# Optimization experiments

Hardware: AMD Instinct MI355X
Metric: run time of the kernel (lower is better)

The kernel has to match this reference:

```python
import jax, jax.numpy as jnp
import numpy as np

B, T, C, H, FF, BOT = 2, 2048, 1024, 16, 4096, 64
D = C // H
EPS = 1e-5

def _ln(x, g, b):
    m = jnp.mean(x, axis=-1, keepdims=True)
    v = jnp.mean(jnp.square(x - m), axis=-1, keepdims=True)
    return (x - m) * jax.lax.rsqrt(v + EPS) * g + b

def setup_inputs() -> dict:
    key = jax.random.key(0)
    ks = jax.random.split(key, 20)
    def lin(k, fan_in, shape):
        return jax.random.normal(k, shape, jnp.float32) * (1.0 / np.sqrt(fan_in))
    inp = {
        "x": jax.random.normal(ks[0], (B, T, C), jnp.float32),
        # causal mask: masked_fill where mask == 0
        "attn_mask": jnp.tril(jnp.ones((T, T), jnp.int32))[None, None, :, :],
        "Wq": lin(ks[1], C, (C, C)), "bq": jnp.zeros((C,), jnp.float32),
        "Wk": lin(ks[2], C, (C, C)), "bk": jnp.zeros((C,), jnp.float32),
        "Wv": lin(ks[3], C, (C, C)), "bv": jnp.zeros((C,), jnp.float32),
        "Wo": lin(ks[4], C, (C, C)), "bo": jnp.zeros((C,), jnp.float32),
        "g1": jnp.ones((C,), jnp.float32), "beta1": jnp.zeros((C,), jnp.float32),
        "g2": jnp.ones((C,), jnp.float32), "beta2": jnp.zeros((C,), jnp.float32),
        "W1": lin(ks[5], C, (C, FF)), "bf1": jnp.zeros((FF,), jnp.float32),
        "W2": lin(ks[6], FF, (FF, C)), "bf2": jnp.zeros((C,), jnp.float32),
        "Wd": lin(ks[7], C, (C, BOT)), "bd": jnp.zeros((BOT,), jnp.float32),
        "Wu": lin(ks[8], BOT, (BOT, C)), "bu": jnp.zeros((C,), jnp.float32),
    }
    return inp

def reference(x, attn_mask, Wq, bq, Wk, bk, Wv, bv, Wo, bo,
              g1, beta1, g2, beta2, W1, bf1, W2, bf2, Wd, bd, Wu, bu):
    # --- attention sublayer ---
    xn = _ln(x, g1, beta1)
    q = (xn @ Wq + bq).reshape(B, T, H, D)
    k = (xn @ Wk + bk).reshape(B, T, H, D)
    v = (xn @ Wv + bv).reshape(B, T, H, D)
    scores = jnp.einsum('bthd,bshd->bhts', q, k) / jnp.sqrt(jnp.float32(D))
    scores = jnp.where(attn_mask == 0, -jnp.inf, scores)
    w = jax.nn.softmax(scores, axis=-1)
    attn = jnp.einsum('bhts,bshd->bthd', w, v).reshape(B, T, C)
    x = x + attn @ Wo + bo
    # --- FFN + adapter sublayer ---
    xn2 = _ln(x, g2, beta2)
    h = jax.nn.relu(xn2 @ W1 + bf1) @ W2 + bf2
    h = h + jax.nn.relu(h @ Wd + bd) @ Wu + bu  # adapter residual
    return x + h
```

## Files before the change

kernel.cpp:

```cpp
#include <hip/hip_runtime.h>
#include <cstdint>
#include <cstddef>

typedef unsigned short u16;
typedef __attribute__((ext_vector_type(4))) short short4v;
typedef __attribute__((ext_vector_type(8))) short short8;
typedef __attribute__((ext_vector_type(4))) float f32x4;

__device__ __forceinline__ float bf2f(u16 h) { return __uint_as_float(((unsigned)h) << 16); }
__device__ __forceinline__ u16 f2bf(float f) {
    unsigned u = __float_as_uint(f);
    unsigned r = (u + 0x7fffu + ((u >> 16) & 1u)) >> 16;
    return (u16)r;
}
__device__ __forceinline__ u16 f2bf_fast(float f) {
    return (u16)((__float_as_uint(f) + 0x8000u) >> 16);
}

__device__ __forceinline__ void gl_lds16(const void* g, void* l) {
    __builtin_amdgcn_global_load_lds((const __attribute__((address_space(1))) void*)g,
                                     (__attribute__((address_space(3))) void*)l, 16, 0, 0);
}

struct Prologue {
    const void* tsrc[8];
    u16* tdst[8];
    int tR[8], tC[8], toff[8];
    const void* psrc[12];
    int poff[12], pn[12];
    int ntrans;
};
__global__ __launch_bounds__(256) void prologue_kernel(Prologue P,
                                                       const unsigned* __restrict__ x,
                                                       int* __restrict__ flag,
                                                       float* __restrict__ pf) {
    __shared__ int cnt[256];
    int c = 0;
    for (int i = threadIdx.x; i < 1024; i += 256) {
        unsigned lo = x[i] & 0xFFFFu;
        unsigned e = (lo >> 7) & 0xFFu;
        c += (e >= 100u && e <= 150u) ? 1 : 0;
    }
    cnt[threadIdx.x] = c;
    __syncthreads();
    for (int s = 128; s > 0; s >>= 1) {
        if (threadIdx.x < s) cnt[threadIdx.x] += cnt[threadIdx.x + s];
        __syncthreads();
    }
    const int bf = (cnt[0] > 512) ? 1 : 0;
    if (blockIdx.x == 0 && threadIdx.x == 0) *flag = bf;

    const int bid = blockIdx.x;
    if (bid >= P.ntrans) {
        const int s = bid - P.ntrans;
        const void* sp = P.psrc[s];
        float* dp = pf + P.poff[s];
        const int n = P.pn[s];
        for (int i = threadIdx.x; i < n; i += 256)
            dp[i] = bf ? bf2f(((const u16*)sp)[i]) : ((const float*)sp)[i];
        return;
    }
    __shared__ u16 tile[32][33];
    int m = 0;
#pragma unroll
    for (int i = 1; i < 8; i++) m = (bid >= P.toff[i]) ? i : m;
    const int local = bid - P.toff[m];
    const int R = P.tR[m], C = P.tC[m];
    const int tilesx = C >> 5;
    const int bx = local % tilesx, by = local / tilesx;
    const void* src = P.tsrc[m];
    u16* dst = P.tdst[m];
    const int tx = threadIdx.x & 31, ty = threadIdx.x >> 5;
#pragma unroll
    for (int i = 0; i < 32; i += 8) {
        size_t idx = (size_t)(by * 32 + ty + i) * C + bx * 32 + tx;
        tile[ty + i][tx] = bf ? ((const u16*)src)[idx] : f2bf(((const float*)src)[idx]);
    }
    __syncthreads();
#pragma unroll
    for (int i = 0; i < 32; i += 8)
        dst[(size_t)(bx * 32 + ty + i) * R + by * 32 + tx] = tile[tx][ty + i];
}

__global__ __launch_bounds__(256) void ln_x_kernel(const void* __restrict__ X,
                                                   const float* __restrict__ G,
                                                   const float* __restrict__ Be,
                                                   u16* __restrict__ Xb,
                                                   u16* __restrict__ Y,
                                                   const int* __restrict__ flag) {
    const int row = blockIdx.x;
    const int tid = threadIdx.x;
    const int lane = tid & 63, wave = tid >> 6;
    u16 vbuf[4];
    if (*flag) {
        *(uint2*)vbuf = *(const uint2*)((const u16*)X + (size_t)row * 1024 + tid * 4);
    } else {
        float4 v = *(const float4*)((const float*)X + (size_t)row * 1024 + tid * 4);
        vbuf[0] = f2bf(v.x); vbuf[1] = f2bf(v.y); vbuf[2] = f2bf(v.z); vbuf[3] = f2bf(v.w);
    }
    *(uint2*)&Xb[(size_t)row * 1024 + tid * 4] = *(uint2*)vbuf;
    float f[4];
    float s = 0.f, sq = 0.f;
#pragma unroll
    for (int j = 0; j < 4; j++) { f[j] = bf2f(vbuf[j]); s += f[j]; sq += f[j] * f[j]; }
#pragma unroll
    for (int m = 1; m < 64; m <<= 1) { s += __shfl_xor(s, m, 64); sq += __shfl_xor(sq, m, 64); }
    __shared__ float rs_[4], rq_[4];
    if (lane == 0) { rs_[wave] = s; rq_[wave] = sq; }
    __syncthreads();
    float S = rs_[0] + rs_[1] + rs_[2] + rs_[3];
    float Q2 = rq_[0] + rq_[1] + rq_[2] + rq_[3];
    float mean = S * (1.f / 1024.f);
    float var = Q2 * (1.f / 1024.f) - mean * mean;
    float rstd = rsqrtf(var + 1e-5f);
    u16 o[4];
#pragma unroll
    for (int j = 0; j < 4; j++) {
        int c2 = tid * 4 + j;
        float y = (f[j] - mean) * rstd * G[c2] + Be[c2];
        o[j] = f2bf(y);
    }
    *(uint2*)&Y[(size_t)row * 1024 + tid * 4] = *(uint2*)o;
}

__global__ __launch_bounds__(256) void ln_kernel(const u16* __restrict__ X,
                                                 const float* __restrict__ G,
                                                 const float* __restrict__ Be,
                                                 u16* __restrict__ Y) {
    const int row = blockIdx.x;
    const int tid = threadIdx.x;
    const int lane = tid & 63, wave = tid >> 6;
    const u16* xr = X + (size_t)row * 1024;
    u16 vbuf[4];
    *(uint2*)vbuf = *(const uint2*)&xr[tid * 4];
    float f[4];
    float s = 0.f, sq = 0.f;
#pragma unroll
    for (int j = 0; j < 4; j++) { f[j] = bf2f(vbuf[j]); s += f[j]; sq += f[j] * f[j]; }
#pragma unroll
    for (int m = 1; m < 64; m <<= 1) { s += __shfl_xor(s, m, 64); sq += __shfl_xor(sq, m, 64); }
    __shared__ float rs_[4], rq_[4];
    if (lane == 0) { rs_[wave] = s; rq_[wave] = sq; }
    __syncthreads();
    float S = rs_[0] + rs_[1] + rs_[2] + rs_[3];
    float Q2 = rq_[0] + rq_[1] + rq_[2] + rq_[3];
    float mean = S * (1.f / 1024.f);
    float var = Q2 * (1.f / 1024.f) - mean * mean;
    float rstd = rsqrtf(var + 1e-5f);
    u16 o[4];
#pragma unroll
    for (int j = 0; j < 4; j++) {
        int c2 = tid * 4 + j;
        float y = (f[j] - mean) * rstd * G[c2] + Be[c2];
        o[j] = f2bf(y);
    }
    *(uint2*)&Y[(size_t)row * 1024 + tid * 4] = *(uint2*)o;
}

template <int TAG>
__global__ __launch_bounds__(512, 4) void gemm128_kernel(const u16* __restrict__ A,
                                                         const u16* __restrict__ Bt,
                                                         const float* __restrict__ bias,
                                                         const u16* __restrict__ res1,
                                                         const u16* __restrict__ res2,
                                                         void* __restrict__ out,
                                                         void* __restrict__ out_k,
                                                         void* __restrict__ out_v,
                                                         int M, int N, int K, int relu, int mode,
                                                         int swz,
                                                         const int* __restrict__ flag) {
    (void)flag; (void)M;
    __shared__ __align__(16) u16 As[2][2][128 * 32];
    __shared__ __align__(16) u16 Bs[2][2][128 * 32];
    const int tid = threadIdx.x;
    const int wave = tid >> 6, lane = tid & 63;
    const int l15 = lane & 15, quad = lane >> 4;
    const int wr = wave & 3, wc = wave >> 2;
    int bx = blockIdx.x, by = blockIdx.y;
    if (swz) {
        const int gx = gridDim.x;
        const int nwg = gx * gridDim.y;
        const int bid = by * gx + bx;
        const int sbid = (bid & 7) * (nwg >> 3) + (bid >> 3);
        bx = sbid % gx;
        by = sbid / gx;
    }
    const int m0 = by * 128, n0 = bx * 128;
    const int nt = K >> 6;

    const int rsub = lane >> 2;
    const int logc = (lane & 3) ^ ((rsub >> 1) & 3);

    auto stage_pair = [&](int t, int kh) {
        const int buf = t & 1;
        const int kk = (t << 6) + (kh << 5) + logc * 8;
        const int roff = wave * 16 + rsub;
        gl_lds16(A + (size_t)(m0 + roff) * K + kk, &As[buf][kh][wave * 512 + lane * 8]);
        gl_lds16(Bt + (size_t)(n0 + roff) * K + kk, &Bs[buf][kh][wave * 512 + lane * 8]);
    };

    f32x4 acc[2][4];
#pragma unroll
    for (int i = 0; i < 2; i++)
#pragma unroll
        for (int j = 0; j < 4; j++) acc[i][j] = (f32x4){0.f, 0.f, 0.f, 0.f};

    stage_pair(0, 0);
    stage_pair(0, 1);
    stage_pair(1, 0);
    asm volatile("s_waitcnt vmcnt(4)" ::: "memory");
    __builtin_amdgcn_s_barrier();

    const int rx = (l15 >> 1) & 3;
    for (int t = 0; t < nt; t++) {
        const int b = t & 1;
#pragma unroll
        for (int ph = 0; ph < 2; ph++) {
            const int kh = ph;
            short8 af[2], bfr[4];
#pragma unroll
            for (int i = 0; i < 2; i++)
                af[i] = *(const short8*)&As[b][kh][(wr * 32 + i * 16 + l15) * 32 +
                                                   ((quad ^ rx) << 3)];
#pragma unroll
            for (int j = 0; j < 4; j++)
                bfr[j] = *(const short8*)&Bs[b][kh][(wc * 64 + j * 16 + l15) * 32 +
                                                    ((quad ^ rx) << 3)];
            if (ph == 0) { if (t + 1 < nt) stage_pair(t + 1, 1); }
            else         { if (t + 2 < nt) stage_pair(t + 2, 0); }
            __builtin_amdgcn_s_setprio(1);
#pragma unroll
            for (int i = 0; i < 2; i++)
#pragma unroll
                for (int j = 0; j < 4; j++)
                    acc[i][j] = __builtin_amdgcn_mfma_f32_16x16x32_bf16(
                        af[i], bfr[j], acc[i][j], 0, 0, 0);
            __builtin_amdgcn_s_setprio(0);
            if (ph == 0) {
                if (t + 1 < nt) { asm volatile("s_waitcnt vmcnt(4)" ::: "memory"); }
                else            { asm volatile("s_waitcnt vmcnt(0)" ::: "memory"); }
            } else {
                if (t + 2 < nt)      { asm volatile("s_waitcnt vmcnt(4)" ::: "memory"); }
                else if (t + 1 < nt) { asm volatile("s_waitcnt vmcnt(2)" ::: "memory"); }
            }
            __builtin_amdgcn_s_barrier();
        }
    }

    if (mode == 2) {
        const int region = n0 >> 10;
        if (region < 2) {
            u16* o = (u16*)(region == 0 ? out : out_k);
#pragma unroll
            for (int j = 0; j < 4; j++) {
                const int col = n0 + wc * 64 + j * 16 + l15;
                const float bv = bias[col];
                const int cl = col & 1023;
#pragma unroll
                for (int i = 0; i < 2; i++) {
                    const int row0 = m0 + wr * 32 + i * 16 + quad * 4;
#pragma unroll
                    for (int r = 0; r < 4; r++)
                        o[(size_t)(row0 + r) * 1024 + cl] = f2bf(acc[i][j][r] + bv);
                }
            }
        } else {
            u16* o = (u16*)out_v;
#pragma unroll
            for (int j = 0; j < 4; j++) {
                const int col = n0 + wc * 64 + j * 16 + l15;
                const float bv = bias[col];
                const int cl = col & 1023;
                const int h = cl >> 6, d = cl & 63;
#pragma unroll
                for (int i = 0; i < 2; i++) {
                    const int row_base = m0 + wr * 32 + i * 16 + quad * 4;
                    const int bb = row_base >> 11, tt = row_base & 2047;
                    u16 pk[4];
#pragma unroll
                    for (int r = 0; r < 4; r++) pk[r] = f2bf(acc[i][j][r] + bv);
                    *(uint2*)&o[(((size_t)bb * 16 + h) * 64 + d) * 2048 + tt] = *(uint2*)pk;
                }
            }
        }
        return;
    }
#pragma unroll
    for (int j = 0; j < 4; j++) {
        const int col = n0 + wc * 64 + j * 16 + l15;
        const float bv = bias ? bias[col] : 0.f;
#pragma unroll
        for (int i = 0; i < 2; i++) {
            const int row0 = m0 + wr * 32 + i * 16 + quad * 4;
#pragma unroll
            for (int r = 0; r < 4; r++) {
                float v = acc[i][j][r] + bv;
                if (relu) v = fmaxf(v, 0.f);
                const size_t idx = (size_t)(row0 + r) * N + col;
                if (res1) v += bf2f(res1[idx]);
                if (res2) v += bf2f(res2[idx]);
                ((u16*)out)[idx] = f2bf(v);
            }
        }
    }
}

template <int TAG>
__global__ __launch_bounds__(512, 2) void gemm256w_kernel(const u16* __restrict__ A,
                                                          const u16* __restrict__ Bt,
                                                          const float* __restrict__ bias,
                                                          void* __restrict__ out,
                                                          int N, int K, int relu) {
    __shared__ __align__(16) u16 As[2][2][256 * 32];
    __shared__ __align__(16) u16 Bs[2][2][256 * 32];
    const int tid = threadIdx.x;
    const int wave = tid >> 6, lane = tid & 63;
    const int l15 = lane & 15, quad = lane >> 4;
    const int wr = wave >> 2, wc = wave & 3;
    const int m0 = blockIdx.y * 256, n0 = blockIdx.x * 256;
    const int nt = K >> 6;

    const int rsub = lane >> 2;
    const int logc = (lane & 3) ^ ((rsub >> 1) & 3);

    auto stage_pair = [&](int t, int kh) {
        const int buf = t & 1;
        const int kk = (t << 6) + (kh << 5) + logc * 8;
        const int r0 = wave * 32 + rsub;
        u16* da = &As[buf][kh][wave * 1024 + lane * 8];
        u16* db = &Bs[buf][kh][wave * 1024 + lane * 8];
        gl_lds16(A + (size_t)(m0 + r0) * K + kk, da);
        gl_lds16(A + (size_t)(m0 + r0 + 16) * K + kk, da + 512);
        gl_lds16(Bt + (size_t)(n0 + r0) * K + kk, db);
        gl_lds16(Bt + (size_t)(n0 + r0 + 16) * K + kk, db + 512);
    };

    f32x4 acc[8][4];
#pragma unroll
    for (int i = 0; i < 8; i++)
#pragma unroll
        for (int j = 0; j < 4; j++) acc[i][j] = (f32x4){0.f, 0.f, 0.f, 0.f};

    stage_pair(0, 0);
    stage_pair(0, 1);
    stage_pair(1, 0);
    asm volatile("s_waitcnt vmcnt(8)" ::: "memory");
    __builtin_amdgcn_s_barrier();

    const int rx = (l15 >> 1) & 3;
    for (int t = 0; t < nt; t++) {
        const int b = t & 1;
#pragma unroll
        for (int ph = 0; ph < 2; ph++) {
            const int kh = ph;
            short8 af[8], bfr[4];
#pragma unroll
            for (int i = 0; i < 8; i++)
                af[i] = *(const short8*)&As[b][kh][(wr * 128 + i * 16 + l15) * 32 +
                                                   ((quad ^ rx) << 3)];
#pragma unroll
            for (int j = 0; j < 4; j++)
                bfr[j] = *(const short8*)&Bs[b][kh][(wc * 64 + j * 16 + l15) * 32 +
                                                    ((quad ^ rx) << 3)];
            if (ph == 0) { if (t + 1 < nt) stage_pair(t + 1, 1); }
            else         { if (t + 2 < nt) stage_pair(t + 2, 0); }
            __builtin_amdgcn_s_setprio(1);
#pragma unroll
            for (int i = 0; i < 8; i++)
#pragma unroll
                for (int j = 0; j < 4; j++)
                    acc[i][j] = __builtin_amdgcn_mfma_f32_16x16x32_bf16(
                        af[i], bfr[j], acc[i][j], 0, 0, 0);
            __builtin_amdgcn_s_setprio(0);
            if (ph == 0) {
                if (t + 1 < nt) { asm volatile("s_waitcnt vmcnt(8)" ::: "memory"); }
                else            { asm volatile("s_waitcnt vmcnt(0)" ::: "memory"); }
            } else {
                if (t + 2 < nt)      { asm volatile("s_waitcnt vmcnt(8)" ::: "memory"); }
                else if (t + 1 < nt) { asm volatile("s_waitcnt vmcnt(4)" ::: "memory"); }
            }
            __builtin_amdgcn_s_barrier();
        }
    }

#pragma unroll
    for (int j = 0; j < 4; j++) {
        const int col = n0 + wc * 64 + j * 16 + l15;
        const float bv = bias ? bias[col] : 0.f;
#pragma unroll
        for (int i = 0; i < 8; i++) {
            const int row0 = m0 + wr * 128 + i * 16 + quad * 4;
#pragma unroll
            for (int r = 0; r < 4; r++) {
                float v = acc[i][j][r] + bv;
                if (relu) v = fmaxf(v, 0.f);
                ((u16*)out)[(size_t)(row0 + r) * N + col] = f2bf(v);
            }
        }
    }
}

template <int TAG>
__global__ __launch_bounds__(512, 2) void gemm128d_kernel(const u16* __restrict__ A,
                                                          const u16* __restrict__ Bt,
                                                          const float* __restrict__ bias,
                                                          const u16* __restrict__ res1,
                                                          void* __restrict__ out,
                                                          int N, int K, int relu, int swz) {
    __shared__ __align__(16) u16 As[2][2][128 * 64];
    __shared__ __align__(16) u16 Bs[2][2][128 * 64];
    const int tid = threadIdx.x;
    const int wave = tid >> 6, lane = tid & 63;
    const int l15 = lane & 15, quad = lane >> 4;
    const int wr = wave & 3, wc = wave >> 2;
    int bx = blockIdx.x, by = blockIdx.y;
    if (swz) {
        const int gx = gridDim.x;
        const int nwg = gx * gridDim.y;
        const int bid = by * gx + bx;
        const int sbid = (bid & 7) * (nwg >> 3) + (bid >> 3);
        bx = sbid % gx;
        by = sbid / gx;
    }
    const int m0 = by * 128, n0 = bx * 128;
    const int nt = K >> 7;

    const int srow = lane >> 3;
    const int logc = (lane & 7) ^ ((lane >> 4) & 3);

    auto stage_pair = [&](int t, int kh) {
        const int buf = t & 1;
        const int kk = (t << 7) + (kh << 6) + logc * 8;
        const int r0 = wave * 16 + srow;
        u16* da = &As[buf][kh][wave * 1024 + lane * 8];
        u16* db = &Bs[buf][kh][wave * 1024 + lane * 8];
        gl_lds16(A + (size_t)(m0 + r0) * K + kk, da);
        gl_lds16(A + (size_t)(m0 + r0 + 8) * K + kk, da + 512);
        gl_lds16(Bt + (size_t)(n0 + r0) * K + kk, db);
        gl_lds16(Bt + (size_t)(n0 + r0 + 8) * K + kk, db + 512);
    };

    f32x4 acc[2][4];
#pragma unroll
    for (int i = 0; i < 2; i++)
#pragma unroll
        for (int j = 0; j < 4; j++) acc[i][j] = (f32x4){0.f, 0.f, 0.f, 0.f};

    stage_pair(0, 0);
    stage_pair(0, 1);
    stage_pair(1, 0);
    asm volatile("s_waitcnt vmcnt(8)" ::: "memory");
    __builtin_amdgcn_s_barrier();

    const int rx = (l15 >> 1) & 3;
    for (int t = 0; t < nt; t++) {
        const int b = t & 1;
#pragma unroll
        for (int ph = 0; ph < 2; ph++) {
            const int kh = ph;
            short8 af[2][2], bfr[4][2];
#pragma unroll
            for (int ks = 0; ks < 2; ks++) {
                const int ck = ((ks << 2) | (quad ^ rx)) << 3;
#pragma unroll
                for (int i = 0; i < 2; i++)
                    af[i][ks] = *(const short8*)&As[b][kh][(wr * 32 + i * 16 + l15) * 64 + ck];
#pragma unroll
                for (int j = 0; j < 4; j++)
                    bfr[j][ks] = *(const short8*)&Bs[b][kh][(wc * 64 + j * 16 + l15) * 64 + ck];
            }
            if (ph == 0) { if (t + 1 < nt) stage_pair(t + 1, 1); }
            else         { if (t + 2 < nt) stage_pair(t + 2, 0); }
            __builtin_amdgcn_s_setprio(1);
#pragma unroll
            for (int ks = 0; ks < 2; ks++)
#pragma unroll
                for (int i = 0; i < 2; i++)
#pragma unroll
                    for (int j = 0; j < 4; j++)
                        acc[i][j] = __builtin_amdgcn_mfma_f32_16x16x32_bf16(
                            af[i][ks], bfr[j][ks], acc[i][j], 0, 0, 0);
            __builtin_amdgcn_s_setprio(0);
            if (ph == 0) {
                if (t + 1 < nt) { asm volatile("s_waitcnt vmcnt(8)" ::: "memory"); }
                else            { asm volatile("s_waitcnt vmcnt(0)" ::: "memory"); }
            } else {
                if (t + 2 < nt)      { asm volatile("s_waitcnt vmcnt(8)" ::: "memory"); }
                else if (t + 1 < nt) { asm volatile("s_waitcnt vmcnt(4)" ::: "memory"); }
            }
            __builtin_amdgcn_s_barrier();
        }
    }

#pragma unroll
    for (int j = 0; j < 4; j++) {
        const int col = n0 + wc * 64 + j * 16 + l15;
        const float bv = bias ? bias[col] : 0.f;
#pragma unroll
        for (int i = 0; i < 2; i++) {
            const int row0 = m0 + wr * 32 + i * 16 + quad * 4;
#pragma unroll
            for (int r = 0; r < 4; r++) {
                float v = acc[i][j][r] + bv;
                if (relu) v = fmaxf(v, 0.f);
                const size_t idx = (size_t)(row0 + r) * N + col;
                if (res1) v += bf2f(res1[idx]);
                ((u16*)out)[idx] = f2bf(v);
            }
        }
    }
}

__global__ __launch_bounds__(512) void adapter_kernel(const u16* __restrict__ hh,
                                                      const u16* __restrict__ x1,
                                                      const u16* __restrict__ WdT,
                                                      const u16* __restrict__ WuT,
                                                      const float* __restrict__ bd,
                                                      const float* __restrict__ bu,
                                                      void* __restrict__ out,
                                                      const int* __restrict__ flag) {
    const int tid = threadIdx.x;
    const int wave = tid >> 6, lane = tid & 63;
    const int l15 = lane & 15, quad = lane >> 4;
    const int r0 = blockIdx.x * 16;

    __shared__ float part[8][16 * 64];
    __shared__ __align__(16) u16 bot_s[16 * 72];

    f32x4 dacc[4];
#pragma unroll
    for (int j = 0; j < 4; j++) dacc[j] = (f32x4){0.f, 0.f, 0.f, 0.f};
    const int kw = wave * 128;
#pragma unroll
    for (int ks = 0; ks < 4; ks++) {
        const int k0 = kw + ks * 32 + quad * 8;
        short8 af = *(const short8*)&hh[(size_t)(r0 + l15) * 1024 + k0];
#pragma unroll
        for (int j = 0; j < 4; j++) {
            short8 bf = *(const short8*)&WdT[(size_t)(j * 16 + l15) * 1024 + k0];
            dacc[j] = __builtin_amdgcn_mfma_f32_16x16x32_bf16(af, bf, dacc[j], 0, 0, 0);
        }
    }
#pragma unroll
    for (int j = 0; j < 4; j++)
#pragma unroll
        for (int r = 0; r < 4; r++)
            part[wave][(quad * 4 + r) * 64 + j * 16 + l15] = dacc[j][r];
    __syncthreads();

    for (int e = tid; e < 1024; e += 512) {
        float s = part[0][e];
#pragma unroll
        for (int w = 1; w < 8; w++) s += part[w][e];
        s += bd[e & 63];
        s = fmaxf(s, 0.f);
        bot_s[(e >> 6) * 72 + (e & 63)] = f2bf(s);
    }
    __syncthreads();

    short8 auf[2];
    auf[0] = *(const short8*)&bot_s[l15 * 72 + quad * 8];
    auf[1] = *(const short8*)&bot_s[l15 * 72 + 32 + quad * 8];
    f32x4 uacc[8];
#pragma unroll
    for (int j = 0; j < 8; j++) uacc[j] = (f32x4){0.f, 0.f, 0.f, 0.f};
#pragma unroll
    for (int j = 0; j < 8; j++) {
        const size_t nb = (size_t)(wave * 128 + j * 16 + l15) * 64;
        short8 b0 = *(const short8*)&WuT[nb + quad * 8];
        short8 b1 = *(const short8*)&WuT[nb + 32 + quad * 8];
        uacc[j] = __builtin_amdgcn_mfma_f32_16x16x32_bf16(auf[0], b0, uacc[j], 0, 0, 0);
        uacc[j] = __builtin_amdgcn_mfma_f32_16x16x32_bf16(auf[1], b1, uacc[j], 0, 0, 0);
    }
    const int f32out = (*flag == 0);
#pragma unroll
    for (int j = 0; j < 8; j++) {
        const int col = wave * 128 + j * 16 + l15;
        const float bv = bu[col];
#pragma unroll
        for (int r = 0; r < 4; r++) {
            const int row = r0 + quad * 4 + r;
            const size_t idx = (size_t)row * 1024 + col;
            float v = uacc[j][r] + bv;
            v += bf2f(hh[idx]);
            v += bf2f(x1[idx]);
            if (f32out) ((float*)out)[idx] = v;
            else ((u16*)out)[idx] = f2bf(v);
        }
    }
}

template <int SPLIT>
__global__ __launch_bounds__(256) void flash_kernel(const u16* __restrict__ Q,
                                                    const u16* __restrict__ Kg,
                                                    const u16* __restrict__ VtG,
                                                    u16* __restrict__ O,
                                                    u16* __restrict__ pO,
                                                    float* __restrict__ pL) {
    const int tid = threadIdx.x;
    const int wave = tid >> 6, lane = tid & 63;
    int qb, ch;
    if (SPLIT) {
        const int i = blockIdx.x;
        if (i < 32)      { qb = 31 - (i >> 2); ch = i & 3; }
        else if (i < 56) { const int j = i - 32; qb = 23 - j / 3; ch = j % 3; }
        else if (i < 72) { const int j = i - 56; qb = 15 - (j >> 1); ch = j & 1; }
        else             { qb = 7 - (i - 72); ch = 0; }
    } else {
        qb = 31 - blockIdx.x; ch = 0;
    }
    const int bh = blockIdx.y;
    const int t0 = qb * 64;
    const int steps = qb + 1;
    const int ktbeg = SPLIT ? ch * 8 : 0;
    const int ktend = SPLIT ? (steps < ktbeg + 8 ? steps : ktbeg + 8) : steps;
    const size_t base = ((size_t)(bh >> 4) * 2048) * 1024 + (size_t)(bh & 15) * 64;
    const size_t basev = (size_t)bh * 64 * 2048;

    __shared__ __align__(16) u16 Ks[2][64 * 64];
    __shared__ __align__(16) u16 Vt[2][64 * 64];
#if !__has_builtin(__builtin_amdgcn_mfma_f32_16x16x16bf16_1k)
    __shared__ __align__(16) u16 Ps[4][16 * 72];
#endif

    const int l15 = lane & 15, quad = lane >> 4;
    const int rmin = t0 + wave * 16;

    short8 qf[2];
    {
        const u16* qp = Q + base + (size_t)(rmin + l15) * 1024 + quad * 8;
        qf[0] = *(const short8*)qp;
        qf[1] = *(const short8*)(qp + 32);
    }

    const int slr = lane >> 3;
    const int sc8 = (lane & 7) ^ slr;
    const int rb = wave * 16;

    auto stage = [&](int kt, int bufi) {
        gl_lds16(Kg + base + (size_t)(kt * 64 + rb + slr) * 1024 + sc8 * 8,
                 &Ks[bufi][rb * 64 + lane * 8]);
        gl_lds16(Kg + base + (size_t)(kt * 64 + rb + 8 + slr) * 1024 + sc8 * 8,
                 &Ks[bufi][(rb + 8) * 64 + lane * 8]);
        gl_lds16(VtG + basev + (size_t)(rb + slr) * 2048 + kt * 64 + sc8 * 8,
                 &Vt[bufi][rb * 64 + lane * 8]);
        gl_lds16(VtG + basev + (size_t)(rb + 8 + slr) * 2048 + kt * 64 + sc8 * 8,
                 &Vt[bufi][(rb + 8) * 64 + lane * 8]);
    };

    float l_part = 0.f;
    f32x4 oacc[4];
#pragma unroll
    for (int jt = 0; jt < 4; jt++) oacc[jt] = (f32x4){0.f, 0.f, 0.f, 0.f};

    const float Cs = 0.125f * 1.44269504f;

    stage(ktbeg, 0);
    __syncthreads();

    for (int kt = ktbeg; kt < ktend; kt++) {
        const int cur = kt & 1;
        if (kt + 1 < ktend) stage(kt + 1, cur ^ 1);

        short8 kf[2][4];
#pragma unroll
        for (int st = 0; st < 2; st++)
#pragma unroll
            for (int j = 0; j < 4; j++)
                kf[st][j] = *(const short8*)&Ks[cur][(j * 16 + l15) * 64 +
                                                     (((st * 4 + quad) ^ (l15 & 7)) * 8)];
#if __has_builtin(__builtin_amdgcn_mfma_f32_16x16x16bf16_1k)
        short4v vf[4][4];
#pragma unroll
        for (int j = 0; j < 4; j++) {
            int k8 = j * 2 + (quad >> 1);
#pragma unroll
            for (int jt = 0; jt < 4; jt++) {
                int d = jt * 16 + l15;
                vf[j][jt] = *(const short4v*)&Vt[cur][d * 64 + ((k8 ^ (d & 7)) * 8) +
                                                      (quad & 1) * 4];
            }
        }
#else
        short8 vf[2][4];
#pragma unroll
        for (int st = 0; st < 2; st++)
#pragma unroll
            for (int jt = 0; jt < 4; jt++) {
                int d = jt * 16 + l15;
                vf[st][jt] = *(const short8*)&Vt[cur][d * 64 + (((st * 4 + quad) ^ (d & 7)) * 8)];
            }
#endif

        f32x4 s[4];
#pragma unroll
        for (int j = 0; j < 4; j++) s[j] = (f32x4){0.f, 0.f, 0.f, 0.f};
#pragma unroll
        for (int st = 0; st < 2; st++)
#pragma unroll
            for (int j = 0; j < 4; j++)
                s[j] = __builtin_amdgcn_mfma_f32_16x16x32_bf16(kf[st][j], qf[st], s[j], 0, 0, 0);

        float lpv[4] = {0.f, 0.f, 0.f, 0.f};
        short4v pj[4];
        if (kt != qb) {
#pragma unroll
            for (int j = 0; j < 4; j++) {
                union { short4v v; u16 u[4]; } pk;
#pragma unroll
                for (int r = 0; r < 4; r++) {
                    float p = __builtin_amdgcn_exp2f(s[j][r] * Cs);
                    lpv[r] += p;
                    pk.u[r] = f2bf_fast(p);
                }
                pj[j] = pk.v;
            }
        } else {
            const int qrow = rmin + l15;
#pragma unroll
            for (int j = 0; j < 4; j++) {
                union { short4v v; u16 u[4]; } pk;
#pragma unroll
                for (int r = 0; r < 4; r++) {
                    float p = __builtin_amdgcn_exp2f(s[j][r] * Cs);
                    int key = kt * 64 + j * 16 + quad * 4 + r;
                    if (key > qrow) p = 0.f;
                    lpv[r] += p;
                    pk.u[r] = f2bf_fast(p);
                }
                pj[j] = pk.v;
            }
        }
        l_part += (lpv[0] + lpv[1]) + (lpv[2] + lpv[3]);

#if __has_builtin(__builtin_amdgcn_mfma_f32_16x16x16bf16_1k)
#pragma unroll
        for (int jt = 0; jt < 4; jt++)
#pragma unroll
            for (int j = 0; j < 4; j++)
                oacc[jt] = __builtin_amdgcn_mfma_f32_16x16x16bf16_1k(pj[j], vf[j][jt],
                                                                     oacc[jt], 0, 0, 0);
#else
        u16* Pw = Ps[wave];
#pragma unroll
        for (int j = 0; j < 4; j++)
            *(short4v*)&Pw[l15 * 72 + j * 16 + quad * 4] = pj[j];
#pragma unroll
        for (int st = 0; st < 2; st++) {
            short8 pf2 = *(const short8*)&Pw[l15 * 72 + st * 32 + quad * 8];
#pragma unroll
            for (int jt = 0; jt < 4; jt++)
                oacc[jt] = __builtin_amdgcn_mfma_f32_16x16x32_bf16(pf2, vf[st][jt],
                                                                  oacc[jt], 0, 0, 0);
        }
#endif
        __syncthreads();
    }

    float lf = l_part;
    lf += __shfl_xor(lf, 16, 64);
    lf += __shfl_xor(lf, 32, 64);

    if (SPLIT && steps > 8) {
        const size_t ib = ((size_t)bh * 24 + (qb - 8)) * 4 + ch;
        u16* po = pO + ib * 4096;
#pragma unroll
        for (int jt = 0; jt < 4; jt++)
#pragma unroll
            for (int r = 0; r < 4; r++)
                po[(wave * 16 + quad * 4 + r) * 64 + jt * 16 + l15] = f2bf(oacc[jt][r]);
        if (quad == 0) pL[ib * 64 + wave * 16 + l15] = lf;
        return;
    }

    {
        float inv[4];
#pragma unroll
        for (int r = 0; r < 4; r++) inv[r] = 1.f / __shfl(lf, quad * 4 + r, 64);
#pragma unroll
        for (int jt = 0; jt < 4; jt++) {
            int d = jt * 16 + l15;
#pragma unroll
            for (int r = 0; r < 4; r++) {
                int t = rmin + quad * 4 + r;
                O[base + (size_t)t * 1024 + d] = f2bf(oacc[jt][r] * inv[r]);
            }
        }
    }
}

__global__ __launch_bounds__(256) void flash_combine_kernel(const u16* __restrict__ pO,
                                                            const float* __restrict__ pL,
                                                            u16* __restrict__ O) {
    const int qj = blockIdx.x;
    const int bh = blockIdx.y;
    const int qb = qj + 8;
    const int nch = (qb >> 3) + 1;
    const int tid = threadIdx.x;
    const int row = tid >> 2;
    const int d0 = (tid & 3) * 16;
    const size_t ib = ((size_t)bh * 24 + qj) * 4;

    float acc[16];
#pragma unroll
    for (int k = 0; k < 16; k++) acc[k] = 0.f;
    float lsum = 0.f;
    for (int c = 0; c < nch; c++) {
        const u16* po = pO + (ib + c) * 4096 + row * 64 + d0;
        u16 pb[16];
        *(uint4*)pb = *(const uint4*)po;
        *(uint4*)(pb + 8) = *(const uint4*)(po + 8);
#pragma unroll
        for (int k = 0; k < 16; k++) acc[k] += bf2f(pb[k]);
        lsum += pL[(ib + c) * 64 + row];
    }
    const float inv = 1.f / lsum;
    u16 o[16];
#pragma unroll
    for (int k = 0; k < 16; k++) o[k] = f2bf(acc[k] * inv);
    const size_t base = ((size_t)(bh >> 4) * 2048) * 1024 + (size_t)(bh & 15) * 64;
    const int t = qb * 64 + row;
    u16* op = &O[base + (size_t)t * 1024 + d0];
    *(uint4*)op = ((uint4*)o)[0];
    *(uint4*)(op + 8) = ((uint4*)o)[1];
}

extern "C" void kernel_launch(void* const* d_in, const int* in_sizes, int n_in,
                              void* d_out, int out_size, void* d_ws, size_t ws_size,
                              hipStream_t stream) {
    (void)in_sizes; (void)n_in; (void)out_size;
    const void* x   = d_in[0];
    const void* Wq  = d_in[2];  const void* bq  = d_in[3];
    const void* Wk  = d_in[4];  const void* bk  = d_in[5];
    const void* Wv  = d_in[6];  const void* bv  = d_in[7];
    const void* Wo  = d_in[8];  const void* bo  = d_in[9];
    const void* g1  = d_in[10]; const void* be1 = d_in[11];
    const void* g2  = d_in[12]; const void* be2 = d_in[13];
    const void* W1  = d_in[14]; const void* bf1 = d_in[15];
    const void* W2  = d_in[16]; const void* bf2 = d_in[17];
    const void* Wd  = d_in[18]; const void* bd  = d_in[19];
    const void* Wu  = d_in[20]; const void* bu  = d_in[21];

    uint8_t* w8 = (uint8_t*)d_ws;
    int* flag = (int*)w8;
    float* pf = (float*)(w8 + 64);
    u16* wsb = (u16*)(w8 + 64 + 65536);

    const size_t M1 = 1024ull * 1024ull;
    u16* WqT = wsb;
    u16* WkT = wsb + 1 * M1;
    u16* WvT = wsb + 2 * M1;
    u16* WoT = wsb + 3 * M1;
    u16* W1T = wsb + 4 * M1;
    u16* W2T = wsb + 8 * M1;
    u16* WdT = wsb + 12 * M1;
    u16* WuT = wsb + 12 * M1 + 65536;
    u16* S0  = wsb + 12 * M1 + 131072;
    u16* Areg = S0;
    u16* Breg = S0 + 4 * M1;
    u16* ff1  = S0;
    u16* Creg = S0 + 16 * M1;
    u16* Dreg = S0 + 20 * M1;
    u16* Ereg = S0 + 24 * M1;
    u16* xb = Areg;
    u16* xn = Breg; u16* attn = Breg;
    u16* q = Creg;  u16* xn2 = Creg;
    u16* kk_ = Dreg; u16* x1 = Dreg;
    u16* VtG = Ereg; u16* hh = Ereg;

    const size_t arena_bytes = (size_t)(64 + 65536) + (40 * M1 + 131072) * 2;
    float* partf = (float*)(w8 + ((arena_bytes + 255) & ~(size_t)255));
    const size_t need = ((arena_bytes + 255) & ~(size_t)255) + 4ull * 4 * M1 * 4;
    const bool sk = ws_size >= need;
    float* flL = partf + 14 * M1;

    float* bqkv_f = pf + 0;
    float* bo_f  = pf + 3072;
    float* bf1_f = pf + 4096;  float* bf2_f = pf + 8192;
    float* bd_f  = pf + 9216;  float* bu_f  = pf + 9280;
    float* g1_f  = pf + 10304; float* be1_f = pf + 11328;
    float* g2_f  = pf + 12352; float* be2_f = pf + 13376;

    Prologue P;
    const void* tsrc[8] = {Wq, Wk, Wv, Wo, W1, W2, Wd, Wu};
    u16* tdst[8] = {WqT, WkT, WvT, WoT, W1T, W2T, WdT, WuT};
    int tR[8] = {1024, 1024, 1024, 1024, 1024, 4096, 1024, 64};
    int tC[8] = {1024, 1024, 1024, 1024, 4096, 1024, 64, 1024};
    int acc_off = 0;
    for (int i = 0; i < 8; i++) {
        P.tsrc[i] = tsrc[i]; P.tdst[i] = tdst[i];
        P.tR[i] = tR[i]; P.tC[i] = tC[i];
        P.toff[i] = acc_off;
        acc_off += (tR[i] >> 5) * (tC[i] >> 5);
    }
    P.ntrans = acc_off;
    const void* psrc[12] = {bq, bk, bv, bo, bf1, bf2, bd, bu, g1, be1, g2, be2};
    int poff[12] = {0, 1024, 2048, 3072, 4096, 8192, 9216, 9280, 10304, 11328, 12352, 13376};
    int pn[12]   = {1024, 1024, 1024, 1024, 4096, 1024, 64, 1024, 1024, 1024, 1024, 1024};
    for (int i = 0; i < 12; i++) { P.psrc[i] = psrc[i]; P.poff[i] = poff[i]; P.pn[i] = pn[i]; }
    prologue_kernel<<<acc_off + 12, 256, 0, stream>>>(P, (const unsigned*)x, flag, pf);

    ln_x_kernel<<<4096, 256, 0, stream>>>(x, g1_f, be1_f, xb, xn, flag);
    gemm128_kernel<0><<<dim3(24, 32), 512, 0, stream>>>(xn, WqT, bqkv_f, nullptr, nullptr,
                                                        q, kk_, VtG, 4096, 3072, 1024, 0, 2, 0, flag);
    if (sk) {
        flash_kernel<1><<<dim3(80, 32), 256, 0, stream>>>(q, kk_, VtG, attn, (u16*)partf, flL);
        flash_combine_kernel<<<dim3(24, 32), 256, 0, stream>>>((const u16*)partf, flL, attn);
    } else {
        flash_kernel<0><<<dim3(32, 32), 256, 0, stream>>>(q, kk_, VtG, attn, nullptr, nullptr);
    }
    gemm128d_kernel<1><<<dim3(8, 32), 512, 0, stream>>>(attn, WoT, bo_f, xb,
                                                        x1, 1024, 1024, 0, 1);
    ln_kernel<<<4096, 256, 0, stream>>>(x1, g2_f, be2_f, xn2);
    gemm256w_kernel<2><<<dim3(16, 16), 512, 0, stream>>>(xn2, W1T, bf1_f,
                                                         ff1, 4096, 1024, 1);
    gemm128d_kernel<3><<<dim3(8, 32), 512, 0, stream>>>(ff1, W2T, bf2_f, nullptr,
                                                        hh, 1024, 4096, 0, 1);
    adapter_kernel<<<256, 512, 0, stream>>>(hh, x1, WdT, WuT, bd_f, bu_f, d_out, flag);
}
```

Before: 403.8 us.

## Pair adjacent query blocks per workgroup to share K/V staging in split flash attention

Adds a 512-thread flash attention kernel in which each workgroup processes two adjacent 64-row query blocks, one per group of four waves, for the same key chunk. Each K/V tile is staged once into LDS and consumed by both halves, which halves global K/V loads and the block count compared with the earlier 80-block split layout. The shorter query block sits idle on the last diagonal step but still joins the barriers. The non-split path becomes a plain non-template kernel.

```diff
diff --git a/kernel.cpp b/kernel.cpp
--- a/kernel.cpp
+++ b/kernel.cpp
@@ -590,30 +590,211 @@
     }
 }
 
-template <int SPLIT>
+__global__ __launch_bounds__(512) void flash_pair_kernel(const u16* __restrict__ Q,
+                                                         const u16* __restrict__ Kg,
+                                                         const u16* __restrict__ VtG,
+                                                         u16* __restrict__ O,
+                                                         u16* __restrict__ pO,
+                                                         float* __restrict__ pL) {
+    const int tid = threadIdx.x;
+    const int wave = tid >> 6, lane = tid & 63;
+    const int half = wave >> 2, w4 = wave & 3;
+    int i = blockIdx.x, c, p;
+    if (i < 16)      { c = 0; p = i; }
+    else if (i < 28) { c = 1; p = i - 16; }
+    else if (i < 36) { c = 2; p = i - 28; }
+    else             { c = 3; p = i - 36; }
+    const int qb = 31 - 2 * p - half;
+    const int bh = blockIdx.y;
+    const int t0 = qb * 64;
+    const int steps = qb + 1;
+    const int ktbeg = c * 8;
+    int ktend = ktbeg + 8; if (steps < ktend) ktend = steps;
+    const int qbA = 31 - 2 * p;
+    int ktend_blk = ktbeg + 8; if (qbA + 1 < ktend_blk) ktend_blk = qbA + 1;
+    const size_t base = ((size_t)(bh >> 4) * 2048) * 1024 + (size_t)(bh & 15) * 64;
+    const size_t basev = (size_t)bh * 64 * 2048;
+
+    __shared__ __align__(16) u16 Ks[2][64 * 64];
+    __shared__ __align__(16) u16 Vt[2][64 * 64];
+#if !__has_builtin(__builtin_amdgcn_mfma_f32_16x16x16bf16_1k)
+    __shared__ __align__(16) u16 Ps[8][16 * 72];
+#endif
+
+    const int l15 = lane & 15, quad = lane >> 4;
+    const int rmin = t0 + w4 * 16;
+
+    short8 qf[2];
+    {
+        const u16* qp = Q + base + (size_t)(rmin + l15) * 1024 + quad * 8;
+        qf[0] = *(const short8*)qp;
+        qf[1] = *(const short8*)(qp + 32);
+    }
+
+    const int slr = lane >> 3;
+    const int sc8 = (lane & 7) ^ slr;
+    const int rb = wave * 8;
+
+    auto stage = [&](int kt, int bufi) {
+        gl_lds16(Kg + base + (size_t)(kt * 64 + rb + slr) * 1024 + sc8 * 8,
+                 &Ks[bufi][rb * 64 + lane * 8]);
+        gl_lds16(VtG + basev + (size_t)(rb + slr) * 2048 + kt * 64 + sc8 * 8,
+                 &Vt[bufi][rb * 64 + lane * 8]);
+    };
+
+    float l_part = 0.f;
+    f32x4 oacc[4];
+#pragma unroll
+    for (int jt = 0; jt < 4; jt++) oacc[jt] = (f32x4){0.f, 0.f, 0.f, 0.f};
+
+    const float Cs = 0.125f * 1.44269504f;
+
+    stage(ktbeg, 0);
+    __syncthreads();
+
+    for (int kt = ktbeg; kt < ktend_blk; kt++) {
+        const int cur = kt & 1;
+        if (kt + 1 < ktend_blk) stage(kt + 1, cur ^ 1);
+
+        if (kt < ktend) {
+            short8 kf[2][4];
+#pragma unroll
+            for (int st = 0; st < 2; st++)
+#pragma unroll
+                for (int j = 0; j < 4; j++)
+                    kf[st][j] = *(const short8*)&Ks[cur][(j * 16 + l15) * 64 +
+                                                         (((st * 4 + quad) ^ (l15 & 7)) * 8)];
+#if __has_builtin(__builtin_amdgcn_mfma_f32_16x16x16bf16_1k)
+            short4v vf[4][4];
+#pragma unroll
+            for (int j = 0; j < 4; j++) {
+                int k8 = j * 2 + (quad >> 1);
+#pragma unroll
+                for (int jt = 0; jt < 4; jt++) {
+                    int d = jt * 16 + l15;
+                    vf[j][jt] = *(const short4v*)&Vt[cur][d * 64 + ((k8 ^ (d & 7)) * 8) +
+                                                          (quad & 1) * 4];
+                }
+            }
+#else
+            short8 vf[2][4];
+#pragma unroll
+            for (int st = 0; st < 2; st++)
+#pragma unroll
+                for (int jt = 0; jt < 4; jt++) {
+                    int d = jt * 16 + l15;
+                    vf[st][jt] = *(const short8*)&Vt[cur][d * 64 + (((st * 4 + quad) ^ (d & 7)) * 8)];
+                }
+#endif
+
+            f32x4 s[4];
+#pragma unroll
+            for (int j = 0; j < 4; j++) s[j] = (f32x4){0.f, 0.f, 0.f, 0.f};
+#pragma unroll
+            for (int st = 0; st < 2; st++)
+#pragma unroll
+                for (int j = 0; j < 4; j++)
+                    s[j] = __builtin_amdgcn_mfma_f32_16x16x32_bf16(kf[st][j], qf[st], s[j], 0, 0, 0);
+
+            float lpv[4] = {0.f, 0.f, 0.f, 0.f};
+            short4v pj[4];
+            if (kt != qb) {
+#pragma unroll
+                for (int j = 0; j < 4; j++) {
+                    union { short4v v; u16 u[4]; } pk;
+#pragma unroll
+                    for (int r = 0; r < 4; r++) {
+                        float pv = __builtin_amdgcn_exp2f(s[j][r] * Cs);
+                        lpv[r] += pv;
+                        pk.u[r] = f2bf_fast(pv);
+                    }
+                    pj[j] = pk.v;
+                }
+            } else {
+                const int qrow = rmin + l15;
+#pragma unroll
+                for (int j = 0; j < 4; j++) {
+                    union { short4v v; u16 u[4]; } pk;
+#pragma unroll
+                    for (int r = 0; r < 4; r++) {
+                        float pv = __builtin_amdgcn_exp2f(s[j][r] * Cs);
+                        int key = kt * 64 + j * 16 + quad * 4 + r;
+                        if (key > qrow) pv = 0.f;
+                        lpv[r] += pv;
+                        pk.u[r] = f2bf_fast(pv);
+                    }
+                    pj[j] = pk.v;
+                }
+            }
+            l_part += (lpv[0] + lpv[1]) + (lpv[2] + lpv[3]);
+
+#if __has_builtin(__builtin_amdgcn_mfma_f32_16x16x16bf16_1k)
+#pragma unroll
+            for (int jt = 0; jt < 4; jt++)
+#pragma unroll
+                for (int j = 0; j < 4; j++)
+                    oacc[jt] = __builtin_amdgcn_mfma_f32_16x16x16bf16_1k(pj[j], vf[j][jt],
+                                                                         oacc[jt], 0, 0, 0);
+#else
+            u16* Pw = Ps[wave];
+#pragma unroll
+            for (int j = 0; j < 4; j++)
+                *(short4v*)&Pw[l15 * 72 + j * 16 + quad * 4] = pj[j];
+#pragma unroll
+            for (int st = 0; st < 2; st++) {
+                short8 pf2 = *(const short8*)&Pw[l15 * 72 + st * 32 + quad * 8];
+#pragma unroll
+                for (int jt = 0; jt < 4; jt++)
+                    oacc[jt] = __builtin_amdgcn_mfma_f32_16x16x32_bf16(pf2, vf[st][jt],
+                                                                      oacc[jt], 0, 0, 0);
+            }
+#endif
+        }
+        __syncthreads();
+    }
+
+    float lf = l_part;
+    lf += __shfl_xor(lf, 16, 64);
+    lf += __shfl_xor(lf, 32, 64);
+
+    if (steps > 8) {
+        const size_t ib = ((size_t)bh * 24 + (qb - 8)) * 4 + c;
+        u16* po = pO + ib * 4096;
+#pragma unroll
+        for (int jt = 0; jt < 4; jt++)
+#pragma unroll
+            for (int r = 0; r < 4; r++)
+                po[(w4 * 16 + quad * 4 + r) * 64 + jt * 16 + l15] = f2bf(oacc[jt][r]);
+        if (quad == 0) pL[ib * 64 + w4 * 16 + l15] = lf;
+        return;
+    }
+
+    {
+        float inv[4];
+#pragma unroll
+        for (int r = 0; r < 4; r++) inv[r] = 1.f / __shfl(lf, quad * 4 + r, 64);
+#pragma unroll
+        for (int jt = 0; jt < 4; jt++) {
+            int d = jt * 16 + l15;
+#pragma unroll
+            for (int r = 0; r < 4; r++) {
+                int t = rmin + quad * 4 + r;
+                O[base + (size_t)t * 1024 + d] = f2bf(oacc[jt][r] * inv[r]);
+            }
+        }
+    }
+}
+
 __global__ __launch_bounds__(256) void flash_kernel(const u16* __restrict__ Q,
                                                     const u16* __restrict__ Kg,
                                                     const u16* __restrict__ VtG,
-                                                    u16* __restrict__ O,
-                                                    u16* __restrict__ pO,
-                                                    float* __restrict__ pL) {
+                                                    u16* __restrict__ O) {
     const int tid = threadIdx.x;
     const int wave = tid >> 6, lane = tid & 63;
-    int qb, ch;
-    if (SPLIT) {
-        const int i = blockIdx.x;
-        if (i < 32)      { qb = 31 - (i >> 2); ch = i & 3; }
-        else if (i < 56) { const int j = i - 32; qb = 23 - j / 3; ch = j % 3; }
-        else if (i < 72) { const int j = i - 56; qb = 15 - (j >> 1); ch = j & 1; }
-        else             { qb = 7 - (i - 72); ch = 0; }
-    } else {
-        qb = 31 - blockIdx.x; ch = 0;
-    }
+    const int qb = 31 - blockIdx.x;
     const int bh = blockIdx.y;
     const int t0 = qb * 64;
     const int steps = qb + 1;
-    const int ktbeg = SPLIT ? ch * 8 : 0;
-    const int ktend = SPLIT ? (steps < ktbeg + 8 ? steps : ktbeg + 8) : steps;
     const size_t base = ((size_t)(bh >> 4) * 2048) * 1024 + (size_t)(bh & 15) * 64;
     const size_t basev = (size_t)bh * 64 * 2048;
 
@@ -655,12 +836,12 @@
 
     const float Cs = 0.125f * 1.44269504f;
 
-    stage(ktbeg, 0);
+    stage(0, 0);
     __syncthreads();
 
-    for (int kt = ktbeg; kt < ktend; kt++) {
+    for (int kt = 0; kt < steps; kt++) {
         const int cur = kt & 1;
-        if (kt + 1 < ktend) stage(kt + 1, cur ^ 1);
+        if (kt + 1 < steps) stage(kt + 1, cur ^ 1);
 
         short8 kf[2][4];
 #pragma unroll
@@ -709,9 +890,9 @@
                 union { short4v v; u16 u[4]; } pk;
 #pragma unroll
                 for (int r = 0; r < 4; r++) {
-                    float p = __builtin_amdgcn_exp2f(s[j][r] * Cs);
-                    lpv[r] += p;
-                    pk.u[r] = f2bf_fast(p);
+                    float pv = __builtin_amdgcn_exp2f(s[j][r] * Cs);
+                    lpv[r] += pv;
+                    pk.u[r] = f2bf_fast(pv);
                 }
                 pj[j] = pk.v;
             }
@@ -722,11 +903,11 @@
                 union { short4v v; u16 u[4]; } pk;
 #pragma unroll
                 for (int r = 0; r < 4; r++) {
-                    float p = __builtin_amdgcn_exp2f(s[j][r] * Cs);
+                    float pv = __builtin_amdgcn_exp2f(s[j][r] * Cs);
                     int key = kt * 64 + j * 16 + quad * 4 + r;
-                    if (key > qrow) p = 0.f;
-                    lpv[r] += p;
-                    pk.u[r] = f2bf_fast(p);
+                    if (key > qrow) pv = 0.f;
+                    lpv[r] += pv;
+                    pk.u[r] = f2bf_fast(pv);
                 }
                 pj[j] = pk.v;
             }
@@ -760,31 +941,16 @@
     float lf = l_part;
     lf += __shfl_xor(lf, 16, 64);
     lf += __shfl_xor(lf, 32, 64);
-
-    if (SPLIT && steps > 8) {
-        const size_t ib = ((size_t)bh * 24 + (qb - 8)) * 4 + ch;
-        u16* po = pO + ib * 4096;
-#pragma unroll
-        for (int jt = 0; jt < 4; jt++)
-#pragma unroll
-            for (int r = 0; r < 4; r++)
-                po[(wave * 16 + quad * 4 + r) * 64 + jt * 16 + l15] = f2bf(oacc[jt][r]);
-        if (quad == 0) pL[ib * 64 + wave * 16 + l15] = lf;
-        return;
-    }
-
-    {
-        float inv[4];
-#pragma unroll
-        for (int r = 0; r < 4; r++) inv[r] = 1.f / __shfl(lf, quad * 4 + r, 64);
-#pragma unroll
-        for (int jt = 0; jt < 4; jt++) {
-            int d = jt * 16 + l15;
-#pragma unroll
-            for (int r = 0; r < 4; r++) {
-                int t = rmin + quad * 4 + r;
-                O[base + (size_t)t * 1024 + d] = f2bf(oacc[jt][r] * inv[r]);
-            }
+    float inv[4];
+#pragma unroll
+    for (int r = 0; r < 4; r++) inv[r] = 1.f / __shfl(lf, quad * 4 + r, 64);
+#pragma unroll
+    for (int jt = 0; jt < 4; jt++) {
+        int d = jt * 16 + l15;
+#pragma unroll
+        for (int r = 0; r < 4; r++) {
+            int t = rmin + quad * 4 + r;
+            O[base + (size_t)t * 1024 + d] = f2bf(oacc[jt][r] * inv[r]);
         }
     }
 }
@@ -904,10 +1070,10 @@
     gemm128_kernel<0><<<dim3(24, 32), 512, 0, stream>>>(xn, WqT, bqkv_f, nullptr, nullptr,
                                                         q, kk_, VtG, 4096, 3072, 1024, 0, 2, 0, flag);
     if (sk) {
-        flash_kernel<1><<<dim3(80, 32), 256, 0, stream>>>(q, kk_, VtG, attn, (u16*)partf, flL);
+        flash_pair_kernel<<<dim3(40, 32), 512, 0, stream>>>(q, kk_, VtG, attn, (u16*)partf, flL);
         flash_combine_kernel<<<dim3(24, 32), 256, 0, stream>>>((const u16*)partf, flL, attn);
     } else {
-        flash_kernel<0><<<dim3(32, 32), 256, 0, stream>>>(q, kk_, VtG, attn, nullptr, nullptr);
+        flash_kernel<<<dim3(32, 32), 256, 0, stream>>>(q, kk_, VtG, attn);
     }
     gemm128d_kernel<1><<<dim3(8, 32), 512, 0, stream>>>(attn, WoT, bo_f, xb,
                                                         x1, 1024, 1024, 0, 1);
```

Result: no change. 396.0 us (median of 2 runs) (-1.9%).
